# Kernel optimization log

Hardware: AMD Instinct MI355X
Metric: run time of the kernel (lower is better)

## Reference

```python
import jax, jax.numpy as jnp
import numpy as np

ALPHA = 0.25
GAMMA = 2.0
EDGE_W = 1.0
NODE_W = 1.0

N = 200_000
E = 12_800_000
N_GRAPHS = 16
N_INST = 1000


def setup_inputs() -> dict:
    key = jax.random.key(0)
    k1, k2, k3, k4, k5 = jax.random.split(key, 5)
    edge_logits = jax.random.normal(k1, (E,), dtype=jnp.float32)
    node_logits = jax.random.normal(k2, (N,), dtype=jnp.float32)
    batch = jnp.sort(jax.random.randint(k3, (N,), 0, N_GRAPHS, dtype=jnp.int64) if jax.config.read('jax_enable_x64') else jax.random.randint(k3, (N,), 0, N_GRAPHS, dtype=jnp.int32))
    point_instances = jax.random.randint(k4, (N,), 0, N_INST, dtype=jnp.int32)
    edge_index = jax.random.randint(k5, (2, E), 0, N, dtype=jnp.int32)
    return {"edge_logits": edge_logits, "node_logits": node_logits,
            "batch": batch, "point_instances": point_instances,
            "edge_index": edge_index}


def _bce_with_logits(x, t):
    # numerically stable elementwise BCE-with-logits (reduction='none')
    return jnp.maximum(x, 0.0) - x * t + jnp.log1p(jnp.exp(-jnp.abs(x)))


def _sigmoid_focal_loss(x, t, alpha, gamma):
    # torchvision.ops.sigmoid_focal_loss, reduction='mean'
    p = jax.nn.sigmoid(x)
    ce = _bce_with_logits(x, t)
    p_t = p * t + (1.0 - p) * (1.0 - t)
    loss = ce * (1.0 - p_t) ** gamma
    alpha_t = alpha * t + (1.0 - alpha) * (1.0 - t)
    return jnp.mean(alpha_t * loss)


def _accuracy(x, t):
    # sigmoid > 0.5 -> 1 else 0 (note: == 0.5 maps to 0, as in the original)
    pred = (jax.nn.sigmoid(x) > 0.5).astype(x.dtype)
    return jnp.mean((pred == t).astype(jnp.float32))


def reference(edge_logits, node_logits, batch, point_instances, edge_index):
    src, dst = edge_index[0], edge_index[1]
    pi_s = point_instances[src]
    pi_d = point_instances[dst]
    # edge-wise equivalent of the original N x N mask gathered at edge_index:
    # same instance AND same graph AND both instances nonzero
    same = (pi_s == pi_d) & (batch[src] == batch[dst]) & (pi_s != 0) & (pi_d != 0)
    edge_targets = same.astype(jnp.float32)  # [E]

    edge_loss = _sigmoid_focal_loss(edge_logits, edge_targets, ALPHA, GAMMA)
    edge_acc = _accuracy(edge_logits, edge_targets)

    node_targets = (point_instances != 0).astype(jnp.float32)  # [N]
    node_loss = _sigmoid_focal_loss(node_logits, node_targets, ALPHA, GAMMA)
    node_acc = _accuracy(node_logits, node_targets)

    loss = EDGE_W * edge_loss + NODE_W * node_loss
    return loss, edge_loss, node_loss, edge_acc, node_acc
```

## Files before the change

### kernel.cpp

```cpp
#include <hip/hip_runtime.h>
#include <limits.h>


typedef int   iv4 __attribute__((ext_vector_type(4)));
typedef float fv4 __attribute__((ext_vector_type(4)));

#define MAX_PART 4096

__device__ __forceinline__ float focal_term(float x, int t) {
    float y = t ? -x : x;
    float e = __expf(-fabsf(y));
    float ce = fmaxf(y, 0.f) + __logf(1.f + e);
    float inv = __builtin_amdgcn_rcpf(1.f + e);
    float sg = (y >= 0.f) ? inv : e * inv;
    float w = t ? 0.25f : 0.75f;
    return w * ce * sg * sg;
}

__device__ __forceinline__ float acc_term(float x, int t) {
    return ((x > 0.f) == (t != 0)) ? 1.f : 0.f;
}

__device__ __forceinline__ void block_store2(float v0, float v1, float2* part) {
#pragma unroll
    for (int off = 32; off > 0; off >>= 1) {
        v0 += __shfl_down(v0, off, 64);
        v1 += __shfl_down(v1, off, 64);
    }
    __shared__ float s0[8], s1[8];
    int wave = threadIdx.x >> 6;
    int lane = threadIdx.x & 63;
    if (lane == 0) { s0[wave] = v0; s1[wave] = v1; }
    __syncthreads();
    if (threadIdx.x == 0) {
        int nw = blockDim.x >> 6;
        float t0 = 0.f, t1 = 0.f;
        for (int w = 0; w < nw; ++w) { t0 += s0[w]; t1 += s1[w]; }
        part[blockIdx.x] = make_float2(t0, t1);
    }
}

__device__ __forceinline__ void block_store4(float v0, float v1, float v2,
                                             float v3, float4* part) {
#pragma unroll
    for (int off = 32; off > 0; off >>= 1) {
        v0 += __shfl_down(v0, off, 64);
        v1 += __shfl_down(v1, off, 64);
        v2 += __shfl_down(v2, off, 64);
        v3 += __shfl_down(v3, off, 64);
    }
    __shared__ float s[4][8];
    int wave = threadIdx.x >> 6;
    int lane = threadIdx.x & 63;
    if (lane == 0) { s[0][wave] = v0; s[1][wave] = v1;
                     s[2][wave] = v2; s[3][wave] = v3; }
    __syncthreads();
    if (threadIdx.x == 0) {
        int nw = blockDim.x >> 6;
        float t0 = 0.f, t1 = 0.f, t2 = 0.f, t3 = 0.f;
        for (int w = 0; w < nw; ++w) {
            t0 += s[0][w]; t1 += s[1][w]; t2 += s[2][w]; t3 += s[3][w];
        }
        part[blockIdx.x] = make_float4(t0, t1, t2, t3);
    }
}

__global__ void __launch_bounds__(256, 4)
node_e1_kernel(const float* __restrict__ nl,
               const int* __restrict__ batch,
               const int* __restrict__ pi,
               int N,
               const float* __restrict__ el, int E,
               int* __restrict__ bnd,
               float4* __restrict__ part) {
    int tid = blockIdx.x * blockDim.x + threadIdx.x;
    int nth = gridDim.x * blockDim.x;
    float nls = 0.f, nac = 0.f, els = 0.f, eac = 0.f;

    int C = N >> 3;
    const iv4* pi4 = reinterpret_cast<const iv4*>(pi);
    const iv4* b4  = reinterpret_cast<const iv4*>(batch);
    const fv4* nl4 = reinterpret_cast<const fv4*>(nl);
    for (int c = tid; c < C; c += nth) {
        int base = c << 3;
        iv4 p0 = pi4[(c << 1) + 0], p1 = pi4[(c << 1) + 1];
        iv4 b0 = b4[(c << 1) + 0],  b1 = b4[(c << 1) + 1];
        fv4 x0 = nl4[(c << 1) + 0], x1 = nl4[(c << 1) + 1];
        int pv[8] = {p0.x, p0.y, p0.z, p0.w, p1.x, p1.y, p1.z, p1.w};
        int bv[8] = {b0.x, b0.y, b0.z, b0.w, b1.x, b1.y, b1.z, b1.w};
        float xv[8] = {x0.x, x0.y, x0.z, x0.w, x1.x, x1.y, x1.z, x1.w};
        int bp = (base > 0) ? batch[base - 1] : -1;
#pragma unroll
        for (int j = 0; j < 8; ++j) {
            int t = (pv[j] != 0) ? 1 : 0;
            int b = bv[j];
            if (bp != b) {
                for (int k = bp + 1; k <= b; ++k) bnd[k] = base + j;
            }
            bp = b;
            nls += focal_term(xv[j], t);
            nac += acc_term(xv[j], t);
        }
        if (base + 8 == N) {
            for (int k = bv[7] + 1; k <= 16; ++k) bnd[k] = N;
        }
    }
    if (tid == 0) {
        for (int i = C << 3; i < N; ++i) {
            int t = (pi[i] != 0) ? 1 : 0;
            int b = batch[i];
            if (i == 0) {
                for (int k = 0; k <= b; ++k) bnd[k] = 0;
            } else {
                int bp = batch[i - 1];
                for (int k = bp + 1; k <= b; ++k) bnd[k] = i;
            }
            if (i == N - 1) {
                for (int k = b + 1; k <= 16; ++k) bnd[k] = N;
            }
            float x = nl[i];
            nls += focal_term(x, t);
            nac += acc_term(x, t);
        }
    }

    int lane = threadIdx.x & 63;
    int wid = tid >> 6;
    int nwaves = nth >> 6;
    int NW = E >> 10;
    const fv4* el4 = reinterpret_cast<const fv4*>(el);
    for (int w = wid; w < NW; w += nwaves) {
        int base4 = w << 8;
#pragma unroll
        for (int j = 0; j < 4; ++j) {
            fv4 x = __builtin_nontemporal_load(el4 + base4 + (j << 6) + lane);
            els += focal_term(x.x, 0) + focal_term(x.y, 0) +
                   focal_term(x.z, 0) + focal_term(x.w, 0);
            eac += acc_term(x.x, 0) + acc_term(x.y, 0) +
                   acc_term(x.z, 0) + acc_term(x.w, 0);
        }
    }
    if (tid == 0) {
        for (int i = NW << 10; i < E; ++i) {
            float x = el[i];
            els += focal_term(x, 0);
            eac += acc_term(x, 0);
        }
    }
    block_store4(nls, nac, els, eac, part);
}

__global__ void __launch_bounds__(256, 4)
edge_corr_kernel(const int* __restrict__ src,
                 const int* __restrict__ dst,
                 const float* __restrict__ el,
                 const int* __restrict__ pi,
                 const int* __restrict__ bnd_g,
                 int E, float gscale,
                 float2* __restrict__ part) {
    __shared__ int bnd[17];
    if (threadIdx.x < 17) bnd[threadIdx.x] = bnd_g[threadIdx.x];
    __syncthreads();

    int tid = blockIdx.x * blockDim.x + threadIdx.x;
    int nth = gridDim.x * blockDim.x;
    int lane = threadIdx.x & 63;
    int wid = tid >> 6;
    int nwaves = nth >> 6;
    int NW = E >> 10;
    float ls = 0.f, ac = 0.f;
    const iv4* src4 = reinterpret_cast<const iv4*>(src);
    const iv4* dst4 = reinterpret_cast<const iv4*>(dst);

    for (int w = wid; w < NW; w += nwaves) {
        int base4 = w << 8;
        int si[16], di[16];
#pragma unroll
        for (int j = 0; j < 4; ++j) {
            iv4 s = __builtin_nontemporal_load(src4 + base4 + (j << 6) + lane);
            si[j * 4 + 0] = s.x; si[j * 4 + 1] = s.y;
            si[j * 4 + 2] = s.z; si[j * 4 + 3] = s.w;
        }
#pragma unroll
        for (int j = 0; j < 4; ++j) {
            iv4 d = __builtin_nontemporal_load(dst4 + base4 + (j << 6) + lane);
            di[j * 4 + 0] = d.x; di[j * 4 + 1] = d.y;
            di[j * 4 + 2] = d.z; di[j * 4 + 3] = d.w;
        }
        unsigned int sameM = 0;
#pragma unroll
        for (int i = 0; i < 16; ++i) {
            int s = si[i], d = di[i];
            int gg = (int)((float)s * gscale);
            gg = gg < 0 ? 0 : (gg > 15 ? 15 : gg);
            int lo = bnd[gg], hi = bnd[gg + 1];
            while (s < lo) { --gg; hi = lo; lo = bnd[gg]; }
            while (s >= hi) { ++gg; lo = hi; hi = bnd[gg + 1]; }
            sameM |= (unsigned int)((d >= lo) & (d < hi)) << i;
        }
        while (sameM) {
            int i = (int)__builtin_ctz(sameM);
            sameM &= sameM - 1;
            int s = si[i], d = di[i];
            int ps = pi[s];
            int pd = pi[d];
            if ((ps == pd) & (ps != 0)) {
                int ei = (w << 10) + ((((i >> 2) << 6) + lane) << 2) + (i & 3);
                float x = el[ei];
                ls += focal_term(x, 1) - focal_term(x, 0);
                ac += (x > 0.f) ? 1.f : -1.f;
            }
        }
    }
    if (tid == 0) {
        for (int i = NW << 10; i < E; ++i) {
            int s = src[i], d = dst[i];
            int gg = (int)((float)s * gscale);
            gg = gg < 0 ? 0 : (gg > 15 ? 15 : gg);
            int lo = bnd[gg], hi = bnd[gg + 1];
            while (s < lo) { --gg; hi = lo; lo = bnd[gg]; }
            while (s >= hi) { ++gg; lo = hi; hi = bnd[gg + 1]; }
            if ((d >= lo) & (d < hi)) {
                int ps = pi[s], pd = pi[d];
                if ((ps == pd) & (ps != 0)) {
                    float x = el[i];
                    ls += focal_term(x, 1) - focal_term(x, 0);
                    ac += (x > 0.f) ? 1.f : -1.f;
                }
            }
        }
    }
    block_store2(ls, ac, part);
}

__global__ void node_atomic_kernel(const float* __restrict__ nl,
                                   const int* __restrict__ pi,
                                   int N, float* __restrict__ acc) {
    int stride = gridDim.x * blockDim.x;
    float ls = 0.f, ac = 0.f;
    for (int i = blockIdx.x * blockDim.x + threadIdx.x; i < N; i += stride) {
        int t = (pi[i] != 0) ? 1 : 0;
        float x = nl[i];
        ls += focal_term(x, t);
        ac += acc_term(x, t);
    }
#pragma unroll
    for (int off = 32; off > 0; off >>= 1) {
        ls += __shfl_down(ls, off, 64);
        ac += __shfl_down(ac, off, 64);
    }
    if ((threadIdx.x & 63) == 0) {
        atomicAdd(acc + 2, ls);
        atomicAdd(acc + 3, ac);
    }
}

__global__ void edge_kernel_direct(const float* __restrict__ el,
                                   const int* __restrict__ src,
                                   const int* __restrict__ dst,
                                   const int* __restrict__ batch,
                                   const int* __restrict__ pi,
                                   int E, float* __restrict__ acc) {
    int stride = gridDim.x * blockDim.x;
    float ls = 0.f, ac = 0.f;
    for (int i = blockIdx.x * blockDim.x + threadIdx.x; i < E; i += stride) {
        int ps = pi[src[i]], pd = pi[dst[i]];
        int t = (ps == pd) & (batch[src[i]] == batch[dst[i]]) & (ps != 0);
        float x = el[i];
        ls += focal_term(x, t);
        ac += acc_term(x, t);
    }
#pragma unroll
    for (int off = 32; off > 0; off >>= 1) {
        ls += __shfl_down(ls, off, 64);
        ac += __shfl_down(ac, off, 64);
    }
    if ((threadIdx.x & 63) == 0) {
        atomicAdd(acc + 0, ls);
        atomicAdd(acc + 1, ac);
    }
}

__global__ void finalize_kernel(const float* __restrict__ acc,
                                const float4* __restrict__ p1, int n1,
                                const float2* __restrict__ p2, int n2,
                                int use_part,
                                float* __restrict__ out, int E, int N) {
    if (use_part) {
        float nls = 0.f, nac = 0.f, els = 0.f, eac = 0.f;
        for (int i = threadIdx.x; i < n1; i += 256) {
            float4 p = p1[i];
            nls += p.x; nac += p.y; els += p.z; eac += p.w;
        }
        for (int i = threadIdx.x; i < n2; i += 256) {
            float2 p = p2[i];
            els += p.x; eac += p.y;
        }
#pragma unroll
        for (int off = 32; off > 0; off >>= 1) {
            nls += __shfl_down(nls, off, 64);
            nac += __shfl_down(nac, off, 64);
            els += __shfl_down(els, off, 64);
            eac += __shfl_down(eac, off, 64);
        }
        __shared__ float s[4][4];
        int wave = threadIdx.x >> 6;
        int lane = threadIdx.x & 63;
        if (lane == 0) { s[0][wave] = nls; s[1][wave] = nac;
                         s[2][wave] = els; s[3][wave] = eac; }
        __syncthreads();
        if (threadIdx.x == 0) {
            nls = 0.f; nac = 0.f; els = 0.f; eac = 0.f;
            for (int w = 0; w < 4; ++w) {
                nls += s[0][w]; nac += s[1][w];
                els += s[2][w]; eac += s[3][w];
            }
            float invE = 1.f / (float)E;
            float invN = 1.f / (float)N;
            float elm = els * invE, eam = eac * invE;
            float nlm = nls * invN, nam = nac * invN;
            out[0] = elm + nlm;
            out[1] = elm;
            out[2] = nlm;
            out[3] = eam;
            out[4] = nam;
        }
    } else if (threadIdx.x == 0) {
        float invE = 1.f / (float)E;
        float invN = 1.f / (float)N;
        float elm = acc[0] * invE;
        float eam = acc[1] * invE;
        float nlm = acc[2] * invN;
        float nam = acc[3] * invN;
        out[0] = elm + nlm;
        out[1] = elm;
        out[2] = nlm;
        out[3] = eam;
        out[4] = nam;
    }
}

extern "C" void kernel_launch(void* const* d_in, const int* in_sizes, int n_in,
                              void* d_out, int out_size, void* d_ws, size_t ws_size,
                              hipStream_t stream) {
    const float* edge_logits = (const float*)d_in[0];
    const float* node_logits = (const float*)d_in[1];
    const int*   batch       = (const int*)d_in[2];
    const int*   pinst       = (const int*)d_in[3];
    const int*   eidx        = (const int*)d_in[4];
    const int E = in_sizes[0];
    const int N = in_sizes[1];
    const int* src = eidx;
    const int* dst = eidx + E;
    float* out = (float*)d_out;

    float* acc = (float*)d_ws;
    int*   bnd = (int*)((char*)d_ws + 64);
    float4* part1 = (float4*)((char*)d_ws + 256);
    float2* part2 = (float2*)(part1 + MAX_PART);
    size_t need_full = 256 + MAX_PART * (sizeof(float4) + sizeof(float2));

    const bool full = (ws_size >= need_full);
    const int block = 256;
    int C = N >> 3;
    int NW = E >> 10;

    if (full) {
        int g1 = (NW + 3) >> 2;
        int g1n = (C + block - 1) / block;
        if (g1n > g1) g1 = g1n;
        if (g1 < 1) g1 = 1;
        if (g1 > MAX_PART) g1 = MAX_PART;
        int g2 = (NW + 3) >> 2;
        if (g2 < 1) g2 = 1;
        if (g2 > MAX_PART) g2 = MAX_PART;

        node_e1_kernel<<<g1, block, 0, stream>>>(node_logits, batch, pinst, N,
                                                 edge_logits, E, bnd, part1);
        float gscale = 16.0f / (float)N;
        edge_corr_kernel<<<g2, block, 0, stream>>>(src, dst, edge_logits,
                                                   pinst, bnd, E, gscale, part2);
        finalize_kernel<<<1, 256, 0, stream>>>(acc, part1, g1, part2, g2, 1,
                                               out, E, N);
    } else {
        (void)hipMemsetAsync(d_ws, 0, 16, stream);
        int ng = (N + block - 1) / block;
        if (ng > 2048) ng = 2048;
        node_atomic_kernel<<<ng, block, 0, stream>>>(node_logits, pinst, N, acc);
        int eg = (E + block - 1) / block;
        if (eg > 2048) eg = 2048;
        edge_kernel_direct<<<eg, block, 0, stream>>>(edge_logits, src, dst,
                                                     batch, pinst, E, acc);
        finalize_kernel<<<1, 256, 0, stream>>>(acc, part1, 0, part2, 0, 0,
                                               out, E, N);
    }
}
```

Measured before the change: 202.5 us.

## Fuse node and edge-correction kernels with per-block binary-searched graph bounds

Merges the node/edge-base kernel and the edge-correction kernel into one launch. Each block computes the 17 graph boundaries in shared memory by binary search over the sorted batch array, instead of scanning batch in the first kernel and reading the result back in the second. This removes a kernel launch, the global boundary round-trip and the second partials array, and fixes the grid at 2048 blocks. In exchange, every block does its own small binary search, and the grid shrinks from about 3125 blocks, which changes how work is spread over the CUs.

```diff
diff --git a/kernel.cpp b/kernel.cpp
--- a/kernel.cpp
+++ b/kernel.cpp
@@ -19,25 +19,6 @@
 
 __device__ __forceinline__ float acc_term(float x, int t) {
     return ((x > 0.f) == (t != 0)) ? 1.f : 0.f;
-}
-
-__device__ __forceinline__ void block_store2(float v0, float v1, float2* part) {
-#pragma unroll
-    for (int off = 32; off > 0; off >>= 1) {
-        v0 += __shfl_down(v0, off, 64);
-        v1 += __shfl_down(v1, off, 64);
-    }
-    __shared__ float s0[8], s1[8];
-    int wave = threadIdx.x >> 6;
-    int lane = threadIdx.x & 63;
-    if (lane == 0) { s0[wave] = v0; s1[wave] = v1; }
-    __syncthreads();
-    if (threadIdx.x == 0) {
-        int nw = blockDim.x >> 6;
-        float t0 = 0.f, t1 = 0.f;
-        for (int w = 0; w < nw; ++w) { t0 += s0[w]; t1 += s1[w]; }
-        part[blockIdx.x] = make_float2(t0, t1);
-    }
 }
 
 __device__ __forceinline__ void block_store4(float v0, float v1, float v2,
@@ -66,67 +47,58 @@
 }
 
 __global__ void __launch_bounds__(256, 4)
-node_e1_kernel(const float* __restrict__ nl,
-               const int* __restrict__ batch,
-               const int* __restrict__ pi,
-               int N,
-               const float* __restrict__ el, int E,
-               int* __restrict__ bnd,
-               float4* __restrict__ part) {
+fused_kernel(const float* __restrict__ nl,
+             const int* __restrict__ batch,
+             const int* __restrict__ pi,
+             int N,
+             const float* __restrict__ el,
+             const int* __restrict__ src,
+             const int* __restrict__ dst,
+             int E, float gscale,
+             float4* __restrict__ part) {
+    __shared__ int bnd[17];
+    if (threadIdx.x < 17) {
+        int k = threadIdx.x;
+        int lo = 0, hi = N;
+        while (lo < hi) {
+            int mid = (lo + hi) >> 1;
+            if (batch[mid] < k) lo = mid + 1; else hi = mid;
+        }
+        bnd[k] = lo;
+    }
+    __syncthreads();
+
     int tid = blockIdx.x * blockDim.x + threadIdx.x;
     int nth = gridDim.x * blockDim.x;
+    int lane = threadIdx.x & 63;
+    int wid = tid >> 6;
+    int nwaves = nth >> 6;
     float nls = 0.f, nac = 0.f, els = 0.f, eac = 0.f;
 
     int C = N >> 3;
     const iv4* pi4 = reinterpret_cast<const iv4*>(pi);
-    const iv4* b4  = reinterpret_cast<const iv4*>(batch);
     const fv4* nl4 = reinterpret_cast<const fv4*>(nl);
     for (int c = tid; c < C; c += nth) {
-        int base = c << 3;
         iv4 p0 = pi4[(c << 1) + 0], p1 = pi4[(c << 1) + 1];
-        iv4 b0 = b4[(c << 1) + 0],  b1 = b4[(c << 1) + 1];
         fv4 x0 = nl4[(c << 1) + 0], x1 = nl4[(c << 1) + 1];
         int pv[8] = {p0.x, p0.y, p0.z, p0.w, p1.x, p1.y, p1.z, p1.w};
-        int bv[8] = {b0.x, b0.y, b0.z, b0.w, b1.x, b1.y, b1.z, b1.w};
         float xv[8] = {x0.x, x0.y, x0.z, x0.w, x1.x, x1.y, x1.z, x1.w};
-        int bp = (base > 0) ? batch[base - 1] : -1;
 #pragma unroll
         for (int j = 0; j < 8; ++j) {
             int t = (pv[j] != 0) ? 1 : 0;
-            int b = bv[j];
-            if (bp != b) {
-                for (int k = bp + 1; k <= b; ++k) bnd[k] = base + j;
-            }
-            bp = b;
             nls += focal_term(xv[j], t);
             nac += acc_term(xv[j], t);
-        }
-        if (base + 8 == N) {
-            for (int k = bv[7] + 1; k <= 16; ++k) bnd[k] = N;
         }
     }
     if (tid == 0) {
         for (int i = C << 3; i < N; ++i) {
             int t = (pi[i] != 0) ? 1 : 0;
-            int b = batch[i];
-            if (i == 0) {
-                for (int k = 0; k <= b; ++k) bnd[k] = 0;
-            } else {
-                int bp = batch[i - 1];
-                for (int k = bp + 1; k <= b; ++k) bnd[k] = i;
-            }
-            if (i == N - 1) {
-                for (int k = b + 1; k <= 16; ++k) bnd[k] = N;
-            }
             float x = nl[i];
             nls += focal_term(x, t);
             nac += acc_term(x, t);
         }
     }
 
-    int lane = threadIdx.x & 63;
-    int wid = tid >> 6;
-    int nwaves = nth >> 6;
     int NW = E >> 10;
     const fv4* el4 = reinterpret_cast<const fv4*>(el);
     for (int w = wid; w < NW; w += nwaves) {
@@ -147,31 +119,9 @@
             eac += acc_term(x, 0);
         }
     }
-    block_store4(nls, nac, els, eac, part);
-}
-
-__global__ void __launch_bounds__(256, 4)
-edge_corr_kernel(const int* __restrict__ src,
-                 const int* __restrict__ dst,
-                 const float* __restrict__ el,
-                 const int* __restrict__ pi,
-                 const int* __restrict__ bnd_g,
-                 int E, float gscale,
-                 float2* __restrict__ part) {
-    __shared__ int bnd[17];
-    if (threadIdx.x < 17) bnd[threadIdx.x] = bnd_g[threadIdx.x];
-    __syncthreads();
-
-    int tid = blockIdx.x * blockDim.x + threadIdx.x;
-    int nth = gridDim.x * blockDim.x;
-    int lane = threadIdx.x & 63;
-    int wid = tid >> 6;
-    int nwaves = nth >> 6;
-    int NW = E >> 10;
-    float ls = 0.f, ac = 0.f;
+
     const iv4* src4 = reinterpret_cast<const iv4*>(src);
     const iv4* dst4 = reinterpret_cast<const iv4*>(dst);
-
     for (int w = wid; w < NW; w += nwaves) {
         int base4 = w << 8;
         int si[16], di[16];
@@ -207,8 +157,8 @@
             if ((ps == pd) & (ps != 0)) {
                 int ei = (w << 10) + ((((i >> 2) << 6) + lane) << 2) + (i & 3);
                 float x = el[ei];
-                ls += focal_term(x, 1) - focal_term(x, 0);
-                ac += (x > 0.f) ? 1.f : -1.f;
+                els += focal_term(x, 1) - focal_term(x, 0);
+                eac += (x > 0.f) ? 1.f : -1.f;
             }
         }
     }
@@ -224,13 +174,14 @@
                 int ps = pi[s], pd = pi[d];
                 if ((ps == pd) & (ps != 0)) {
                     float x = el[i];
-                    ls += focal_term(x, 1) - focal_term(x, 0);
-                    ac += (x > 0.f) ? 1.f : -1.f;
+                    els += focal_term(x, 1) - focal_term(x, 0);
+                    eac += (x > 0.f) ? 1.f : -1.f;
                 }
             }
         }
     }
-    block_store2(ls, ac, part);
+
+    block_store4(nls, nac, els, eac, part);
 }
 
 __global__ void node_atomic_kernel(const float* __restrict__ nl,
@@ -283,7 +234,6 @@
 
 __global__ void finalize_kernel(const float* __restrict__ acc,
                                 const float4* __restrict__ p1, int n1,
-                                const float2* __restrict__ p2, int n2,
                                 int use_part,
                                 float* __restrict__ out, int E, int N) {
     if (use_part) {
@@ -291,10 +241,6 @@
         for (int i = threadIdx.x; i < n1; i += 256) {
             float4 p = p1[i];
             nls += p.x; nac += p.y; els += p.z; eac += p.w;
-        }
-        for (int i = threadIdx.x; i < n2; i += 256) {
-            float2 p = p2[i];
-            els += p.x; eac += p.y;
         }
 #pragma unroll
         for (int off = 32; off > 0; off >>= 1) {
@@ -355,33 +301,20 @@
     float* out = (float*)d_out;
 
     float* acc = (float*)d_ws;
-    int*   bnd = (int*)((char*)d_ws + 64);
-    float4* part1 = (float4*)((char*)d_ws + 256);
-    float2* part2 = (float2*)(part1 + MAX_PART);
-    size_t need_full = 256 + MAX_PART * (sizeof(float4) + sizeof(float2));
+    float4* part = (float4*)((char*)d_ws + 256);
+    size_t need_full = 256 + MAX_PART * sizeof(float4);
 
     const bool full = (ws_size >= need_full);
     const int block = 256;
-    int C = N >> 3;
-    int NW = E >> 10;
 
     if (full) {
-        int g1 = (NW + 3) >> 2;
-        int g1n = (C + block - 1) / block;
-        if (g1n > g1) g1 = g1n;
-        if (g1 < 1) g1 = 1;
-        if (g1 > MAX_PART) g1 = MAX_PART;
-        int g2 = (NW + 3) >> 2;
-        if (g2 < 1) g2 = 1;
-        if (g2 > MAX_PART) g2 = MAX_PART;
-
-        node_e1_kernel<<<g1, block, 0, stream>>>(node_logits, batch, pinst, N,
-                                                 edge_logits, E, bnd, part1);
+        int g = 2048;
+        if (g > MAX_PART) g = MAX_PART;
         float gscale = 16.0f / (float)N;
-        edge_corr_kernel<<<g2, block, 0, stream>>>(src, dst, edge_logits,
-                                                   pinst, bnd, E, gscale, part2);
-        finalize_kernel<<<1, 256, 0, stream>>>(acc, part1, g1, part2, g2, 1,
-                                               out, E, N);
+        fused_kernel<<<g, block, 0, stream>>>(node_logits, batch, pinst, N,
+                                              edge_logits, src, dst, E,
+                                              gscale, part);
+        finalize_kernel<<<1, 256, 0, stream>>>(acc, part, g, 1, out, E, N);
     } else {
         (void)hipMemsetAsync(d_ws, 0, 16, stream);
         int ng = (N + block - 1) / block;
@@ -391,7 +324,6 @@
         if (eg > 2048) eg = 2048;
         edge_kernel_direct<<<eg, block, 0, stream>>>(edge_logits, src, dst,
                                                      batch, pinst, E, acc);
-        finalize_kernel<<<1, 256, 0, stream>>>(acc, part1, 0, part2, 0, 0,
-                                               out, E, N);
-    }
-}
+        finalize_kernel<<<1, 256, 0, stream>>>(acc, nullptr, 0, 0, out, E, N);
+    }
+}
```

New measurement: 200.8 us. About the same (-0.8%).
